# Kernel tuning notes

Measured on AMD Instinct MI355X. Metric: run time of the kernel, lower is better.

The kernel has to match this reference:

```python
import jax, jax.numpy as jnp
import numpy as np

B, S, D, H = 2, 2048, 1024, 16
HD = D // H  # head_dim = 64
ROPE_BASE = 10000.0


def setup_inputs() -> dict:
    key = jax.random.key(0)
    ks = jax.random.split(key, 5)
    scale = 1.0 / np.sqrt(D)
    return {
        "x": jax.random.normal(ks[0], (B, S, D), dtype=jnp.float32),
        "Wq": jax.random.normal(ks[1], (D, D), dtype=jnp.float32) * scale,
        "Wk": jax.random.normal(ks[2], (D, D), dtype=jnp.float32) * scale,
        "Wv": jax.random.normal(ks[3], (D, D), dtype=jnp.float32) * scale,
        "Wo": jax.random.normal(ks[4], (D, D), dtype=jnp.float32) * scale,
    }


def _rotate_half(x):
    x1, x2 = x[..., : HD // 2], x[..., HD // 2:]
    return jnp.concatenate((-x2, x1), axis=-1)


def _rope_cos_sin(seq_len):
    inv_freq = 1.0 / (ROPE_BASE ** (jnp.arange(0, HD, 2, dtype=jnp.float32) / HD))
    t = jnp.arange(seq_len, dtype=jnp.float32)
    freqs = jnp.outer(t, inv_freq)          # [S, HD/2]
    emb = jnp.concatenate((freqs, freqs), -1)  # [S, HD]
    return jnp.cos(emb), jnp.sin(emb)


def reference(x, Wq, Wk, Wv, Wo):
    # projections (torch Linear: y = x @ W.T), split heads -> [B, H, S, HD]
    def proj(W):
        return (x @ W.T).reshape(B, S, H, HD).transpose(0, 2, 1, 3)

    q, k, v = proj(Wq), proj(Wk), proj(Wv)

    cos, sin = _rope_cos_sin(S)  # [S, HD] each, broadcast over B, H
    q = q * cos + _rotate_half(q) * sin
    k = k * cos + _rotate_half(k) * sin

    scale = 1.0 / np.sqrt(HD)
    scores = jnp.einsum("bhsd,bhtd->bhst", q, k) * scale  # [B,H,S,S]
    attn = jax.nn.softmax(scores, axis=-1)
    out = jnp.einsum("bhst,bhtd->bhsd", attn, v)           # [B,H,S,HD]
    out = out.transpose(0, 2, 1, 3).reshape(B, S, D)
    return out @ Wo.T
```

## Files before the change

### kernel.cpp

```cpp
#include <hip/hip_runtime.h>
#include <hip/hip_bf16.h>
#include <math.h>
#include <stdint.h>

typedef __bf16 bf16;
typedef __bf16 bf16x8 __attribute__((ext_vector_type(8)));
typedef __bf16 bf16x4 __attribute__((ext_vector_type(4)));
typedef float  f32x4  __attribute__((ext_vector_type(4)));

#define MFMA16(a,b,c) __builtin_amdgcn_mfma_f32_16x16x32_bf16((a),(b),(c),0,0,0)

static constexpr int kB  = 2;
static constexpr int kS  = 2048;
static constexpr int kD  = 1024;
static constexpr int kH  = 16;
static constexpr int kHD = 64;
static constexpr int kM  = kB * kS;
static constexpr float kExpC = 0.125f * 1.44269504f;

__global__ void cvt_all(const float* __restrict__ x,
                        const float* __restrict__ wq, const float* __restrict__ wk,
                        const float* __restrict__ wv, const float* __restrict__ wo,
                        bf16* __restrict__ xb,
                        bf16* __restrict__ wqb, bf16* __restrict__ wkb,
                        bf16* __restrict__ wvb, bf16* __restrict__ wob,
                        float2* __restrict__ rtab)
{
  const int i = blockIdx.x * 256 + threadIdx.x;
  const int NX4 = (kM * kD) / 4;
  const int NW4 = (kD * kD) / 4;
  if (i >= NX4 + 4 * NW4) {
    const int idx = i - (NX4 + 4 * NW4);
    const int s = idx >> 5, d = idx & 31;
    const float f = exp2f(-(float)d * 0.4152410118609203f);
    float sn, cs;
    sincosf((float)s * f, &sn, &cs);
    rtab[idx] = make_float2(cs, sn);
    return;
  }
  const float* src; bf16* dst; int off;
  if (i < NX4) { src = x; dst = xb; off = i; }
  else {
    const int j = i - NX4;
    const int seg = j >> 18;
    off = j & (NW4 - 1);
    src = (seg == 0) ? wq : (seg == 1) ? wk : (seg == 2) ? wv : wo;
    dst = (seg == 0) ? wqb : (seg == 1) ? wkb : (seg == 2) ? wvb : wob;
  }
  const float4 v = ((const float4*)src)[off];
  bf16x4 o = { (bf16)v.x, (bf16)v.y, (bf16)v.z, (bf16)v.w };
  ((bf16x4*)dst)[off] = o;
}

__device__ __forceinline__ void gemm_core_128(
    const bf16* __restrict__ A, const bf16* __restrict__ Bw,
    int m0, int n0, int K, bf16* aT, bf16* bT, f32x4 acc[4][4])
{
  const int t = threadIdx.x, lane = t & 63, wave = t >> 6;
  const int wm = wave >> 1, wn = wave & 1;
  const int srow = lane >> 2;
  const int scol = (lane & 3) * 8;
  const bf16* ga0 = A  + (size_t)(m0 + wave * 16 + srow) * K + scol;
  const bf16* ga1 = ga0 + (size_t)64 * K;
  const bf16* gb0 = Bw + (size_t)(n0 + wave * 16 + srow) * K + scol;
  const bf16* gb1 = gb0 + (size_t)64 * K;
  bf16* const wa0 = aT + wave * 512 + lane * 8;
  bf16* const wb0 = bT + wave * 512 + lane * 8;

  bf16x8 ra0 = *(const bf16x8*)ga0;
  bf16x8 ra1 = *(const bf16x8*)ga1;
  bf16x8 rb0 = *(const bf16x8*)gb0;
  bf16x8 rb1 = *(const bf16x8*)gb1;

  for (int k0 = 0; k0 < K; k0 += 32) {
    const int kn = (k0 + 32 < K) ? (k0 + 32) : 0;
    const bf16x8 na0 = *(const bf16x8*)(ga0 + kn);
    const bf16x8 na1 = *(const bf16x8*)(ga1 + kn);
    const bf16x8 nb0 = *(const bf16x8*)(gb0 + kn);
    const bf16x8 nb1 = *(const bf16x8*)(gb1 + kn);
    __syncthreads();
    *(bf16x8*)wa0 = ra0;  *(bf16x8*)(wa0 + 2048) = ra1;
    *(bf16x8*)wb0 = rb0;  *(bf16x8*)(wb0 + 2048) = rb1;
    __syncthreads();
    bf16x8 af[4], bfr[4];
#pragma unroll
    for (int i = 0; i < 4; ++i) {
      af[i]  = *(const bf16x8*)(aT + (wm * 64 + i * 16 + (lane & 15)) * 32 + (lane >> 4) * 8);
      bfr[i] = *(const bf16x8*)(bT + (wn * 64 + i * 16 + (lane & 15)) * 32 + (lane >> 4) * 8);
    }
#pragma unroll
    for (int i = 0; i < 4; ++i)
#pragma unroll
      for (int j = 0; j < 4; ++j)
        acc[i][j] = MFMA16(af[i], bfr[j], acc[i][j]);
    ra0 = na0; ra1 = na1; rb0 = nb0; rb1 = nb1;
  }
}

__global__ __launch_bounds__(256) void proj_qkv(
    const bf16* __restrict__ xb,
    const bf16* __restrict__ wqb, const bf16* __restrict__ wkb, const bf16* __restrict__ wvb,
    bf16* __restrict__ Qb, bf16* __restrict__ Kb, bf16* __restrict__ Vt,
    const float2* __restrict__ rtab)
{
  __shared__ __align__(16) bf16 aT[4096];
  __shared__ __align__(16) bf16 bT[4096];
  __shared__ __align__(16) bf16 vtr[2 * 64 * 136];
  const int z = blockIdx.z;
  const bf16* Ww = (z == 0) ? wqb : (z == 1) ? wkb : wvb;
  const int m0 = blockIdx.x * 128, n0 = blockIdx.y * 128;
  f32x4 acc[4][4] = {};
  gemm_core_128(xb, Ww, m0, n0, kD, aT, bT, acc);

  const int lane = threadIdx.x & 63, wave = threadIdx.x >> 6;
  const int wm = wave >> 1, wn = wave & 1, quad = lane >> 4, lc = lane & 15;
  const int hh = (n0 >> 6) + wn;
  if (z == 2) {
#pragma unroll
    for (int i = 0; i < 4; ++i)
#pragma unroll
      for (int j = 0; j < 4; ++j) {
        bf16x4 p;
#pragma unroll
        for (int r = 0; r < 4; ++r) p[r] = (bf16)acc[i][j][r];
        *(bf16x4*)&vtr[(wn * 64 + j * 16 + lc) * 136 + wm * 64 + i * 16 + quad * 4] = p;
      }
    __syncthreads();
    const int t = threadIdx.x;
    const int row = t >> 1;
    const int sh = (t & 1) * 64;
    const int bidx = m0 >> 11;
    const int hh2 = (n0 >> 6) + (row >> 6);
    const int d = row & 63;
    bf16* dst = Vt + ((size_t)(bidx * kH + hh2) * kHD + d) * kS + (m0 & 2047) + sh;
#pragma unroll
    for (int u = 0; u < 8; ++u)
      *(uint4*)(dst + u * 8) = *(const uint4*)&vtr[row * 136 + sh + u * 8];
  } else {
    bf16* Op = (z == 0) ? Qb : Kb;
    const float f = (z == 0) ? kExpC : 1.0f;
#pragma unroll
    for (int j = 0; j < 2; ++j) {
      const int d = j * 16 + lc;
#pragma unroll
      for (int i = 0; i < 4; ++i)
#pragma unroll
        for (int r = 0; r < 4; ++r) {
          const int m = m0 + wm * 64 + i * 16 + quad * 4 + r;
          const int bidx = m >> 11, s = m & 2047;
          const float2 cs = rtab[s * 32 + d];
          const float v0 = acc[i][j][r], v1 = acc[i][j + 2][r];
          bf16* dst = Op + ((size_t)(bidx * kH + hh) * kS + s) * kHD;
          dst[d]      = (bf16)((v0 * cs.x - v1 * cs.y) * f);
          dst[d + 32] = (bf16)((v1 * cs.x + v0 * cs.y) * f);
        }
    }
  }
}

__global__ __launch_bounds__(256, 2) void attn(
    const bf16* __restrict__ Qb, const bf16* __restrict__ Kb,
    const bf16* __restrict__ Vt, bf16* __restrict__ Ob)
{
  __shared__ __align__(16) bf16 kT[128 * 72];
  __shared__ __align__(16) bf16 vT[64 * 136];
  const int t = threadIdx.x, lane = t & 63, wave = t >> 6;
  const int quad = lane >> 4, lc = lane & 15;
  const int bid = blockIdx.x;
  const int qt = (bid >> 3) & 15;
  const int bh = (bid & 7) * 4 + (bid >> 7);
  const size_t base = (size_t)bh * kS * kHD;
  const bf16* Qp = Qb + base + (size_t)qt * 128 * kHD;
  const bf16* Kp = Kb + base;
  const bf16* Vp = Vt + base;

  bf16x8 qf[2][2];
#pragma unroll
  for (int tm = 0; tm < 2; ++tm)
#pragma unroll
    for (int ks = 0; ks < 2; ++ks)
      qf[tm][ks] = *(const bf16x8*)(Qp + (wave * 32 + tm * 16 + lc) * kHD + ks * 32 + quad * 8);

  f32x4 oacc[2][4] = {};
  f32x4 lacc[2] = {};
  const bf16 one = (bf16)1.0f;
  const bf16x8 ones = { one, one, one, one, one, one, one, one };

  const int srow = t >> 1, shalf = (t & 1) * 32;
  const int vd = t >> 2, vc = t & 3;

  for (int kt = 0; kt < kS / 128; ++kt) {
    __syncthreads();
    {
      const bf16* ksrc = Kp + (size_t)(kt * 128 + srow) * kHD + shalf;
#pragma unroll
      for (int u = 0; u < 4; ++u)
        *(uint4*)&kT[srow * 72 + shalf + u * 8] = *(const uint4*)(ksrc + u * 8);
      const bf16* vsrc = Vp + (size_t)vd * kS + kt * 128 + vc * 32;
#pragma unroll
      for (int u = 0; u < 4; ++u)
        *(uint4*)&vT[vd * 136 + vc * 32 + u * 8] = *(const uint4*)(vsrc + u * 8);
    }
    __syncthreads();

    bf16x8 kf[8][2];
#pragma unroll
    for (int nk = 0; nk < 8; ++nk)
#pragma unroll
      for (int ks = 0; ks < 2; ++ks)
        kf[nk][ks] = *(const bf16x8*)&kT[(nk * 16 + lc) * 72 + ks * 32 + quad * 8];

    bf16x8 pfrag[2][4];
#pragma unroll
    for (int tm = 0; tm < 2; ++tm) {
      f32x4 sc[8] = {};
#pragma unroll
      for (int nk = 0; nk < 8; ++nk) {
        sc[nk] = MFMA16(kf[nk][0], qf[tm][0], sc[nk]);
        sc[nk] = MFMA16(kf[nk][1], qf[tm][1], sc[nk]);
      }
#pragma unroll
      for (int kp = 0; kp < 4; ++kp) {
        bf16x8 p;
#pragma unroll
        for (int j = 0; j < 4; ++j) {
          p[j]     = (bf16)__builtin_amdgcn_exp2f(sc[2 * kp][j]);
          p[j + 4] = (bf16)__builtin_amdgcn_exp2f(sc[2 * kp + 1][j]);
        }
        pfrag[tm][kp] = p;
      }
    }

#pragma unroll
    for (int kp = 0; kp < 4; ++kp)
#pragma unroll
      for (int tm = 0; tm < 2; ++tm)
        lacc[tm] = MFMA16(pfrag[tm][kp], ones, lacc[tm]);

#pragma unroll
    for (int nd = 0; nd < 4; ++nd)
#pragma unroll
      for (int kp = 0; kp < 4; ++kp) {
        const bf16x4 lo = *(const bf16x4*)&vT[(nd * 16 + lc) * 136 + kp * 32 + quad * 4];
        const bf16x4 hi = *(const bf16x4*)&vT[(nd * 16 + lc) * 136 + kp * 32 + 16 + quad * 4];
        const bf16x8 vfr = __builtin_shufflevector(lo, hi, 0, 1, 2, 3, 4, 5, 6, 7);
#pragma unroll
        for (int tm = 0; tm < 2; ++tm)
          oacc[tm][nd] = MFMA16(pfrag[tm][kp], vfr, oacc[tm][nd]);
      }
  }

  const int b = bh >> 4, h = bh & 15;
#pragma unroll
  for (int tm = 0; tm < 2; ++tm)
#pragma unroll
    for (int r = 0; r < 4; ++r) {
      const float inv = 1.0f / lacc[tm][r];
      const int s = qt * 128 + wave * 32 + tm * 16 + quad * 4 + r;
      bf16* dst = Ob + ((size_t)(b * kS + s)) * kD + h * kHD;
#pragma unroll
      for (int nd = 0; nd < 4; ++nd)
        dst[nd * 16 + lc] = (bf16)(oacc[tm][nd][r] * inv);
    }
}

__global__ __launch_bounds__(256) void out_proj(
    const bf16* __restrict__ Ab, const bf16* __restrict__ wob, float* __restrict__ Cout)
{
  __shared__ __align__(16) bf16 aT[4096];
  __shared__ __align__(16) bf16 bT[4096];
  const int m0 = blockIdx.x * 128, n0 = blockIdx.y * 128;
  f32x4 acc[4][4] = {};
  gemm_core_128(Ab, wob, m0, n0, kD, aT, bT, acc);
  const int lane = threadIdx.x & 63, wave = threadIdx.x >> 6;
  const int wm = wave >> 1, wn = wave & 1, quad = lane >> 4, lc = lane & 15;
#pragma unroll
  for (int i = 0; i < 4; ++i)
#pragma unroll
    for (int r = 0; r < 4; ++r) {
      const int m = m0 + wm * 64 + i * 16 + quad * 4 + r;
#pragma unroll
      for (int j = 0; j < 4; ++j)
        Cout[(size_t)m * kD + n0 + wn * 64 + j * 16 + lc] = acc[i][j][r];
    }
}

extern "C" void kernel_launch(void* const* d_in, const int* in_sizes, int n_in,
                              void* d_out, int out_size, void* d_ws, size_t ws_size,
                              hipStream_t stream)
{
  const float* x  = (const float*)d_in[0];
  const float* wq = (const float*)d_in[1];
  const float* wk = (const float*)d_in[2];
  const float* wv = (const float*)d_in[3];
  const float* wo = (const float*)d_in[4];
  float* out = (float*)d_out;

  char* ws = (char*)d_ws;
  const size_t MB = 1024 * 1024;
  if (ws_size < 57 * MB) return;
  bf16* xb  = (bf16*)(ws + 0 * MB);
  bf16* wqb = (bf16*)(ws + 8 * MB);
  bf16* wkb = (bf16*)(ws + 10 * MB);
  bf16* wvb = (bf16*)(ws + 12 * MB);
  bf16* wob = (bf16*)(ws + 14 * MB);
  bf16* Qb  = (bf16*)(ws + 16 * MB);
  bf16* Kb  = (bf16*)(ws + 24 * MB);
  bf16* Ob  = (bf16*)(ws + 40 * MB);
  float2* rtab = (float2*)(ws + 48 * MB);
  bf16* Vtp = (bf16*)(ws + 49 * MB);

  cvt_all<<<8448, 256, 0, stream>>>(x, wq, wk, wv, wo, xb, wqb, wkb, wvb, wob, rtab);
  proj_qkv<<<dim3(32, 8, 3), 256, 0, stream>>>(xb, wqb, wkb, wvb, Qb, Kb, Vtp, rtab);
  attn<<<dim3(512), 256, 0, stream>>>(Qb, Kb, Vtp, Ob);
  out_proj<<<dim3(32, 8), 256, 0, stream>>>(Ob, wob, out);
}
```

Measured before the change: 180.6 us.

## Double-buffer GEMM tiles with direct global-to-LDS loads and shrink V transpose buffer

The shared projection GEMM core now uses the global_load_lds builtin to load A and B tiles straight into LDS. It double-buffers them so the next K-slice is fetched while MFMAs run on the current one, which drops one of the two barriers per iteration and the register staging. The V-transpose epilogue reuses the GEMM shared buffer in two passes with a narrower stride, which cuts the kernel's LDS footprint. Launch bounds now request 4 blocks per CU. The design depends on the async LDS loads being complete before each barrier, and the 4-block bound may pressure registers.

```diff
diff --git a/kernel.cpp b/kernel.cpp
--- a/kernel.cpp
+++ b/kernel.cpp
@@ -17,6 +17,12 @@
 static constexpr int kHD = 64;
 static constexpr int kM  = kB * kS;
 static constexpr float kExpC = 0.125f * 1.44269504f;
+
+__device__ __forceinline__ void gl_lds16(const bf16* g, bf16* l) {
+  __builtin_amdgcn_global_load_lds(
+      (const __attribute__((address_space(1))) unsigned int*)g,
+      (__attribute__((address_space(3))) unsigned int*)l, 16, 0, 0);
+}
 
 __global__ void cvt_all(const float* __restrict__ x,
                         const float* __restrict__ wq, const float* __restrict__ wk,
@@ -54,7 +60,7 @@
 
 __device__ __forceinline__ void gemm_core_128(
     const bf16* __restrict__ A, const bf16* __restrict__ Bw,
-    int m0, int n0, int K, bf16* aT, bf16* bT, f32x4 acc[4][4])
+    int m0, int n0, int K, bf16* smem, f32x4 acc[4][4])
 {
   const int t = threadIdx.x, lane = t & 63, wave = t >> 6;
   const int wm = wave >> 1, wn = wave & 1;
@@ -64,24 +70,27 @@
   const bf16* ga1 = ga0 + (size_t)64 * K;
   const bf16* gb0 = Bw + (size_t)(n0 + wave * 16 + srow) * K + scol;
   const bf16* gb1 = gb0 + (size_t)64 * K;
-  bf16* const wa0 = aT + wave * 512 + lane * 8;
-  bf16* const wb0 = bT + wave * 512 + lane * 8;
-
-  bf16x8 ra0 = *(const bf16x8*)ga0;
-  bf16x8 ra1 = *(const bf16x8*)ga1;
-  bf16x8 rb0 = *(const bf16x8*)gb0;
-  bf16x8 rb1 = *(const bf16x8*)gb1;
-
+  const int woff = wave * 512;
+
+  {
+    bf16* lb = smem;
+    gl_lds16(ga0, lb + woff);
+    gl_lds16(ga1, lb + 2048 + woff);
+    gl_lds16(gb0, lb + 4096 + woff);
+    gl_lds16(gb1, lb + 6144 + woff);
+  }
+  int cur = 0;
   for (int k0 = 0; k0 < K; k0 += 32) {
-    const int kn = (k0 + 32 < K) ? (k0 + 32) : 0;
-    const bf16x8 na0 = *(const bf16x8*)(ga0 + kn);
-    const bf16x8 na1 = *(const bf16x8*)(ga1 + kn);
-    const bf16x8 nb0 = *(const bf16x8*)(gb0 + kn);
-    const bf16x8 nb1 = *(const bf16x8*)(gb1 + kn);
     __syncthreads();
-    *(bf16x8*)wa0 = ra0;  *(bf16x8*)(wa0 + 2048) = ra1;
-    *(bf16x8*)wb0 = rb0;  *(bf16x8*)(wb0 + 2048) = rb1;
-    __syncthreads();
+    if (k0 + 32 < K) {
+      bf16* lb = smem + (cur ^ 1) * 8192;
+      gl_lds16(ga0 + k0 + 32, lb + woff);
+      gl_lds16(ga1 + k0 + 32, lb + 2048 + woff);
+      gl_lds16(gb0 + k0 + 32, lb + 4096 + woff);
+      gl_lds16(gb1 + k0 + 32, lb + 6144 + woff);
+    }
+    const bf16* aT = smem + cur * 8192;
+    const bf16* bT = aT + 4096;
     bf16x8 af[4], bfr[4];
 #pragma unroll
     for (int i = 0; i < 4; ++i) {
@@ -93,49 +102,56 @@
 #pragma unroll
       for (int j = 0; j < 4; ++j)
         acc[i][j] = MFMA16(af[i], bfr[j], acc[i][j]);
-    ra0 = na0; ra1 = na1; rb0 = nb0; rb1 = nb1;
-  }
-}
-
-__global__ __launch_bounds__(256) void proj_qkv(
+    cur ^= 1;
+  }
+}
+
+__global__ __launch_bounds__(256, 4) void proj_qkv(
     const bf16* __restrict__ xb,
     const bf16* __restrict__ wqb, const bf16* __restrict__ wkb, const bf16* __restrict__ wvb,
     bf16* __restrict__ Qb, bf16* __restrict__ Kb, bf16* __restrict__ Vt,
     const float2* __restrict__ rtab)
 {
-  __shared__ __align__(16) bf16 aT[4096];
-  __shared__ __align__(16) bf16 bT[4096];
-  __shared__ __align__(16) bf16 vtr[2 * 64 * 136];
+  __shared__ __align__(16) bf16 smem[16384];
   const int z = blockIdx.z;
   const bf16* Ww = (z == 0) ? wqb : (z == 1) ? wkb : wvb;
   const int m0 = blockIdx.x * 128, n0 = blockIdx.y * 128;
   f32x4 acc[4][4] = {};
-  gemm_core_128(xb, Ww, m0, n0, kD, aT, bT, acc);
+  gemm_core_128(xb, Ww, m0, n0, kD, smem, acc);
 
   const int lane = threadIdx.x & 63, wave = threadIdx.x >> 6;
   const int wm = wave >> 1, wn = wave & 1, quad = lane >> 4, lc = lane & 15;
   const int hh = (n0 >> 6) + wn;
   if (z == 2) {
-#pragma unroll
-    for (int i = 0; i < 4; ++i)
-#pragma unroll
-      for (int j = 0; j < 4; ++j) {
-        bf16x4 p;
-#pragma unroll
-        for (int r = 0; r < 4; ++r) p[r] = (bf16)acc[i][j][r];
-        *(bf16x4*)&vtr[(wn * 64 + j * 16 + lc) * 136 + wm * 64 + i * 16 + quad * 4] = p;
-      }
     __syncthreads();
     const int t = threadIdx.x;
     const int row = t >> 1;
-    const int sh = (t & 1) * 64;
+    const int coff = (t & 1) * 32;
     const int bidx = m0 >> 11;
     const int hh2 = (n0 >> 6) + (row >> 6);
     const int d = row & 63;
-    bf16* dst = Vt + ((size_t)(bidx * kH + hh2) * kHD + d) * kS + (m0 & 2047) + sh;
-#pragma unroll
-    for (int u = 0; u < 8; ++u)
-      *(uint4*)(dst + u * 8) = *(const uint4*)&vtr[row * 136 + sh + u * 8];
+    bf16* vtr = smem;
+#pragma unroll
+    for (int p = 0; p < 2; ++p) {
+      if (p) __syncthreads();
+      if (wm == p) {
+#pragma unroll
+        for (int i = 0; i < 4; ++i)
+#pragma unroll
+          for (int j = 0; j < 4; ++j) {
+            bf16x4 pk;
+#pragma unroll
+            for (int r = 0; r < 4; ++r) pk[r] = (bf16)acc[i][j][r];
+            *(bf16x4*)&vtr[(wn * 64 + j * 16 + lc) * 72 + i * 16 + quad * 4] = pk;
+          }
+      }
+      __syncthreads();
+      bf16* dst = Vt + ((size_t)(bidx * kH + hh2) * kHD + d) * kS
+                     + (m0 & 2047) + p * 64 + coff;
+#pragma unroll
+      for (int u = 0; u < 4; ++u)
+        *(uint4*)(dst + u * 8) = *(const uint4*)&vtr[row * 72 + coff + u * 8];
+    }
   } else {
     bf16* Op = (z == 0) ? Qb : Kb;
     const float f = (z == 0) ? kExpC : 1.0f;
@@ -264,14 +280,13 @@
     }
 }
 
-__global__ __launch_bounds__(256) void out_proj(
+__global__ __launch_bounds__(256, 4) void out_proj(
     const bf16* __restrict__ Ab, const bf16* __restrict__ wob, float* __restrict__ Cout)
 {
-  __shared__ __align__(16) bf16 aT[4096];
-  __shared__ __align__(16) bf16 bT[4096];
+  __shared__ __align__(16) bf16 smem[16384];
   const int m0 = blockIdx.x * 128, n0 = blockIdx.y * 128;
   f32x4 acc[4][4] = {};
-  gemm_core_128(Ab, wob, m0, n0, kD, aT, bT, acc);
+  gemm_core_128(Ab, wob, m0, n0, kD, smem, acc);
   const int lane = threadIdx.x & 63, wave = threadIdx.x >> 6;
   const int wm = wave >> 1, wn = wave & 1, quad = lane >> 4, lc = lane & 15;
 #pragma unroll
```

Result: no change. 178.6 us (-1.1%).
